# Performance work log

Hardware: AMD Instinct MI355X
Metric: run time of the kernel (lower is better)

Reference implementation:

```python
import jax, jax.numpy as jnp
import numpy as np

B, T, N, U = 64, 8, 1000, 64
IN_DIM = 1
F = IN_DIM + U          # per-node concat feature size = 65
K = 3                   # num_matrices = max_diffusion_step(2) * n_supports(1) + 1


def _scaled_laplacian(A):
    # calculate_scaled_laplacian from DCRNN preprocessing (filter_type='laplacian')
    A = np.maximum(A, A.T)
    d = A.sum(1)
    d_is = np.where(d > 0, d ** -0.5, 0.0)
    L = np.eye(N, dtype=np.float32) - (d_is[:, None] * A * d_is[None, :])
    lmax = float(np.linalg.eigvalsh(L).max())
    return ((2.0 / lmax) * L - np.eye(N, dtype=np.float32)).astype(np.float32)


def setup_inputs() -> dict:
    key = jax.random.key(0)
    ks = jax.random.split(key, 14)
    # sparse-ish random symmetric adjacency -> scaled Laplacian support
    mask = np.asarray(jax.random.uniform(ks[0], (N, N))) < 0.01
    A = (np.abs(np.asarray(jax.random.normal(ks[1], (N, N)))) * mask).astype(np.float32)
    support = jnp.asarray(_scaled_laplacian(A))

    s = 0.1
    inp = {
        'inputs': jax.random.normal(ks[2], (B, T, N), dtype=jnp.float32),
        'support': support,
        'enc_W_ru': jax.random.normal(ks[3], (F * K, 2 * U), dtype=jnp.float32) * s,
        'enc_b_ru': jnp.ones((2 * U,), jnp.float32),  # bias_start=1.0 in DCGRUCell
        'enc_W_c': jax.random.normal(ks[4], (F * K, U), dtype=jnp.float32) * s,
        'enc_b_c': jnp.zeros((U,), jnp.float32),
        'dec_W_ru': jax.random.normal(ks[5], (F * K, 2 * U), dtype=jnp.float32) * s,
        'dec_b_ru': jnp.ones((2 * U,), jnp.float32),
        'dec_W_c': jax.random.normal(ks[6], (F * K, U), dtype=jnp.float32) * s,
        'dec_b_c': jnp.zeros((U,), jnp.float32),
        'W_proj': jax.random.normal(ks[7], (U, 1), dtype=jnp.float32) * s,
        'b_proj': jnp.zeros((1,), jnp.float32),
    }
    return inp


def _gconv(S, x, h, W, b):
    # x: (B,N,in_dim), h: (B,N,U) -> diffusion conv with Chebyshev recurrence, K=3
    x0 = jnp.concatenate([x, h], axis=-1)                 # (B,N,F)
    x1 = jnp.einsum('mn,bnf->bmf', S, x0)
    x2 = 2.0 * jnp.einsum('mn,bnf->bmf', S, x1) - x0
    xs = jnp.stack([x0, x1, x2], axis=-1)                 # (B,N,F,K) -> matches torch f*K+k layout
    xs = xs.reshape(xs.shape[0], xs.shape[1], -1)         # (B,N,F*K)
    return jnp.einsum('bnf,fo->bno', xs, W) + b


def _dcgru_cell(S, x, h, W_ru, b_ru, W_c, b_c):
    ru = jax.nn.sigmoid(_gconv(S, x, h, W_ru, b_ru))      # (B,N,2U)
    r, u = jnp.split(ru, 2, axis=-1)
    c = jnp.tanh(_gconv(S, x, r * h, W_c, b_c))
    return u * h + (1.0 - u) * c


def reference(inputs, support, enc_W_ru, enc_b_ru, enc_W_c, enc_b_c,
              dec_W_ru, dec_b_ru, dec_W_c, dec_b_c, W_proj, b_proj):
    b, t, n = inputs.shape
    xseq = jnp.transpose(inputs, (1, 0, 2))[..., None]    # (T,B,N,1)
    h0 = jnp.zeros((b, n, U), inputs.dtype)

    def step(h, xt):
        h_new = _dcgru_cell(support, xt, h, enc_W_ru, enc_b_ru, enc_W_c, enc_b_c)
        return h_new, None

    h_enc, _ = jax.lax.scan(step, h0, xseq)
    # decoder: horizon=1, GO symbol = zeros
    go = jnp.zeros((b, n, 1), inputs.dtype)
    h_dec = _dcgru_cell(support, go, h_enc, dec_W_ru, dec_b_ru, dec_W_c, dec_b_c)
    out = (jnp.einsum('bnu,uo->bno', h_dec, W_proj) + b_proj)[..., 0]  # (B,N)
    return out
```

## Files before the change

### kernel.cpp

```cpp
#include <hip/hip_runtime.h>
#include <hip/hip_bf16.h>

namespace {
constexpr int B  = 64;
constexpr int T  = 8;
constexpr int N  = 1000;
constexpr int U  = 64;
constexpr int R  = B * N;
constexpr int RS = 256;
constexpr int CSR_CAP = 65536;
}

typedef short bf16x8 __attribute__((ext_vector_type(8)));
typedef float f32x4  __attribute__((ext_vector_type(4)));
typedef unsigned short u16;

__device__ __forceinline__ float bf2f(u16 x) {
  unsigned u = ((unsigned)x) << 16;
  float f; __builtin_memcpy(&f, &u, 4); return f;
}
__device__ __forceinline__ u16 f2bf(float f) {
  unsigned u; __builtin_memcpy(&u, &f, 4);
  u += 0x7FFFu + ((u >> 16) & 1u);
  return (u16)(u >> 16);
}


__global__ __launch_bounds__(256) void k_count(const float* __restrict__ S,
                                               int* __restrict__ rowptr) {
  int lane = threadIdx.x & 63;
  int m = blockIdx.x * 4 + (threadIdx.x >> 6);
  int c = 0;
  for (int n = lane; n < N; n += 64) c += (S[m * N + n] != 0.f) ? 1 : 0;
  for (int off = 32; off; off >>= 1) c += __shfl_down(c, off, 64);
  if (lane == 0) rowptr[m + 1] = c;
}

__global__ __launch_bounds__(1024) void k_scan(int* __restrict__ rowptr) {
  __shared__ int sm[1024];
  int t = threadIdx.x;
  sm[t] = (t < N) ? rowptr[t + 1] : 0;
  __syncthreads();
  for (int off = 1; off < 1024; off <<= 1) {
    int v = sm[t];
    int a = (t >= off) ? sm[t - off] : 0;
    __syncthreads();
    sm[t] = v + a;
    __syncthreads();
  }
  if (t < N) rowptr[t + 1] = sm[t];
  if (t == 0) rowptr[0] = 0;
}

__global__ __launch_bounds__(256) void k_fill(const float* __restrict__ S,
                                              const int* __restrict__ rowptr,
                                              int* __restrict__ cols,
                                              float* __restrict__ vals) {
  int lane = threadIdx.x & 63;
  int m = blockIdx.x * 4 + (threadIdx.x >> 6);
  int base = rowptr[m];
  for (int n0 = 0; n0 < N; n0 += 64) {
    int n = n0 + lane;
    float v = (n < N) ? S[m * N + n] : 0.f;
    bool nz = (v != 0.f);
    unsigned long long mask = __ballot(nz);
    int pos = base + (int)__popcll(mask & ((1ull << lane) - 1ull));
    if (nz && pos < CSR_CAP) { cols[pos] = n; vals[pos] = v; }
    base += (int)__popcll(mask);
  }
}


__global__ __launch_bounds__(256) void k_xt(const float* __restrict__ inp,
                                            float* __restrict__ xT) {
  __shared__ float tile[64][65];
  const int t  = blockIdx.y;
  const int n0 = blockIdx.x * 64;
  const int lx = threadIdx.x & 63;
  const int ly = threadIdx.x >> 6;
  for (int bb = ly; bb < 64; bb += 4) {
    int n = n0 + lx;
    tile[bb][lx] = (n < N) ? inp[(bb * T + t) * N + n] : 0.f;
  }
  __syncthreads();
  for (int nn = ly; nn < 64; nn += 4) {
    int n = n0 + nn;
    if (n < N) xT[((size_t)t * N + n) * 64 + lx] = tile[lx][nn];
  }
}


__global__ __launch_bounds__(64) void k_sspmv(const int* __restrict__ rowptr,
                                              const int* __restrict__ cols,
                                              const float* __restrict__ vals,
                                              const float* __restrict__ in,
                                              const float* __restrict__ sub,
                                              float* __restrict__ out, int cheb) {
  const int m = blockIdx.x, b = threadIdx.x;
  const size_t toff = (size_t)blockIdx.y * R;
  float acc = 0.f;
  for (int j = rowptr[m]; j < rowptr[m + 1]; ++j)
    acc = fmaf(vals[j], in[toff + cols[j] * 64 + b], acc);
  if (cheb) acc = 2.f * acc - sub[toff + m * 64 + b];
  out[toff + m * 64 + b] = acc;
}


__global__ __launch_bounds__(256) void k_wprep(
    const float* __restrict__ w0, const float* __restrict__ w1,
    const float* __restrict__ w2, const float* __restrict__ w3,
    u16* __restrict__ o0, u16* __restrict__ o1,
    u16* __restrict__ o2, u16* __restrict__ o3) {
  const float* W; u16* O; int ncol;
  switch (blockIdx.y) {
    case 0:  W = w0; O = o0; ncol = 128; break;
    case 1:  W = w1; O = o1; ncol = 64;  break;
    case 2:  W = w2; O = o2; ncol = 128; break;
    default: W = w3; O = o3; ncol = 64;  break;
  }
  int idx = blockIdx.x * 256 + threadIdx.x;
  if (idx >= ncol * RS) return;
  int o = idx / RS, kp = idx - o * RS;
  float v = 0.f;
  if (kp < 192)      v = W[(((kp & 63) + 1) * 3 + (kp >> 6)) * ncol + o];
  else if (kp < 195) v = W[(kp - 192) * ncol + o];
  O[idx] = f2bf(v);
}


__global__ __launch_bounds__(256) void k_zseg(u16* __restrict__ A) {
  int idx = blockIdx.x * 256 + threadIdx.x;
  int r = idx >> 3, q = idx & 7;
  bf16x8 z = {0, 0, 0, 0, 0, 0, 0, 0};
  *(bf16x8*)(A + (size_t)r * RS + q * 8) = z;
}


__global__ __launch_bounds__(256) void k_spv(
    const int* __restrict__ rowptr, const int* __restrict__ cols,
    const float* __restrict__ vals,
    const u16* __restrict__ in, const u16* __restrict__ sub,
    u16* __restrict__ out,
    const float* __restrict__ xs0, const float* __restrict__ xs1,
    const float* __restrict__ xs2,
    u16* __restrict__ scA, u16* __restrict__ scB, int xmode) {
  const int chunk = blockIdx.x;
  const int m = blockIdx.y * 4 + (threadIdx.x >> 6);
  const int l = threadIdx.x & 63;
  const int b = chunk * 8 + (l >> 3);
  const int cg = (l & 7) * 8;
  const int s = rowptr[m], e = rowptr[m + 1];

  float acc[8];
#pragma unroll
  for (int i = 0; i < 8; ++i) acc[i] = 0.f;

  int j = s;
  for (; j + 7 < e; j += 8) {
    float vv[8]; bf16x8 qq[8];
#pragma unroll
    for (int u8 = 0; u8 < 8; ++u8) {
      vv[u8] = vals[j + u8];
      qq[u8] = *(const bf16x8*)(in + ((size_t)cols[j + u8] * 64 + b) * RS + cg);
    }
#pragma unroll
    for (int i = 0; i < 8; ++i) {
      float a = acc[i];
#pragma unroll
      for (int u8 = 0; u8 < 8; ++u8) a = fmaf(vv[u8], bf2f((u16)qq[u8][i]), a);
      acc[i] = a;
    }
  }
  for (; j + 3 < e; j += 4) {
    const float v0 = vals[j],     v1 = vals[j + 1];
    const float v2 = vals[j + 2], v3 = vals[j + 3];
    bf16x8 q0 = *(const bf16x8*)(in + ((size_t)cols[j]     * 64 + b) * RS + cg);
    bf16x8 q1 = *(const bf16x8*)(in + ((size_t)cols[j + 1] * 64 + b) * RS + cg);
    bf16x8 q2 = *(const bf16x8*)(in + ((size_t)cols[j + 2] * 64 + b) * RS + cg);
    bf16x8 q3 = *(const bf16x8*)(in + ((size_t)cols[j + 3] * 64 + b) * RS + cg);
#pragma unroll
    for (int i = 0; i < 8; ++i)
      acc[i] = fmaf(v3, bf2f((u16)q3[i]),
               fmaf(v2, bf2f((u16)q2[i]),
               fmaf(v1, bf2f((u16)q1[i]),
               fmaf(v0, bf2f((u16)q0[i]), acc[i]))));
  }
  for (; j < e; ++j) {
    const float v = vals[j];
    bf16x8 q = *(const bf16x8*)(in + ((size_t)cols[j] * 64 + b) * RS + cg);
#pragma unroll
    for (int i = 0; i < 8; ++i) acc[i] = fmaf(v, bf2f((u16)q[i]), acc[i]);
  }

  const size_t ro = ((size_t)m * 64 + b) * RS + cg;
  if (sub) {
    bf16x8 sb = *(const bf16x8*)(sub + ro);
#pragma unroll
    for (int i = 0; i < 8; ++i) acc[i] = 2.f * acc[i] - bf2f((u16)sb[i]);
  }
  bf16x8 o;
#pragma unroll
  for (int i = 0; i < 8; ++i) o[i] = (short)f2bf(acc[i]);
  *(bf16x8*)(out + ro) = o;

  if (xmode && (l & 7) == 0) {
    const int r = m * 64 + b;
    u16 s0v = 0, s1v = 0, s2v = 0;
    if (xmode == 1) { s0v = f2bf(xs0[r]); s1v = f2bf(xs1[r]); s2v = f2bf(xs2[r]); }
    const size_t o2 = (size_t)r * RS + 192;
    scA[o2] = s0v; scA[o2 + 1] = s1v; scA[o2 + 2] = s2v;
    scB[o2] = s0v; scB[o2 + 1] = s1v; scB[o2 + 2] = s2v;
  }
}


template <int EPI>
__global__ __launch_bounds__(128) void k_mg2(
    const u16* __restrict__ A, const u16* __restrict__ Wt,
    const float* __restrict__ bias,
    u16* __restrict__ outA, u16* __restrict__ ubuf,
    float* __restrict__ hbuf) {
  __shared__ u16 Wl[64 * 128];
  const int chunk = blockIdx.x;
  const int ob = EPI ? 0 : blockIdx.z * 64;
  const int wv = threadIdx.x >> 6;
  const int n0 = EPI ? (blockIdx.y * 4 + wv * 2) : (blockIdx.y * 8 + wv * 4);
  const int l  = threadIdx.x & 63;
  const int lr = l & 15, lk = l >> 4;
  const int bphys = chunk * 8 + (lr & 7);
  const int tc = threadIdx.x & 15, tr0 = threadIdx.x >> 4;

  const size_t ra0 = ((size_t)(n0 + (lr >> 3)) * 64 + bphys) * RS + lk * 8;
  const size_t ra1 = ra0 + 2 * 64 * RS;

  f32x4 acc[2][4];
#pragma unroll
  for (int i = 0; i < 2; ++i)
#pragma unroll
    for (int j = 0; j < 4; ++j) acc[i][j] = (f32x4){0.f, 0.f, 0.f, 0.f};

  for (int r = tr0; r < 64; r += 8)
    *(bf16x8*)(Wl + r * 128 + ((tc ^ (r & 7)) * 8)) =
        *(const bf16x8*)(Wt + (size_t)(ob + r) * RS + tc * 8);
  __syncthreads();
#pragma unroll
  for (int ks = 0; ks < 4; ++ks) {
    bf16x8 a0 = *(const bf16x8*)(A + ra0 + ks * 32);
    bf16x8 a1;
    if (!EPI) a1 = *(const bf16x8*)(A + ra1 + ks * 32);
#pragma unroll
    for (int cb = 0; cb < 4; ++cb) {
      const int wrow = cb * 16 + lr;
      bf16x8 bb = *(const bf16x8*)(Wl + wrow * 128 +
                                   (((ks * 4 + lk) ^ (wrow & 7)) * 8));
      acc[0][cb] = __builtin_amdgcn_mfma_f32_16x16x32_bf16(a0, bb, acc[0][cb], 0, 0, 0);
      if (!EPI)
        acc[1][cb] = __builtin_amdgcn_mfma_f32_16x16x32_bf16(a1, bb, acc[1][cb], 0, 0, 0);
    }
  }
  __syncthreads();
  if (tc < 12)
    for (int r = tr0; r < 64; r += 8)
      *(bf16x8*)(Wl + r * 128 + ((tc ^ (r & 7)) * 8)) =
          *(const bf16x8*)(Wt + (size_t)(ob + r) * RS + 128 + tc * 8);
  __syncthreads();
#pragma unroll
  for (int ks = 4; ks < 7; ++ks) {
    bf16x8 a0 = *(const bf16x8*)(A + ra0 + ks * 32);
    bf16x8 a1;
    if (!EPI) a1 = *(const bf16x8*)(A + ra1 + ks * 32);
#pragma unroll
    for (int cb = 0; cb < 4; ++cb) {
      const int wrow = cb * 16 + lr;
      bf16x8 bb = *(const bf16x8*)(Wl + wrow * 128 +
                                   ((((ks - 4) * 4 + lk) ^ (wrow & 7)) * 8));
      acc[0][cb] = __builtin_amdgcn_mfma_f32_16x16x32_bf16(a0, bb, acc[0][cb], 0, 0, 0);
      if (!EPI)
        acc[1][cb] = __builtin_amdgcn_mfma_f32_16x16x32_bf16(a1, bb, acc[1][cb], 0, 0, 0);
    }
  }

#pragma unroll
  for (int mf = 0; mf < (EPI ? 1 : 2); ++mf)
#pragma unroll
    for (int cb = 0; cb < 4; ++cb) {
      const int col = ob + cb * 16 + lr;
      const float bs = bias[col];
#pragma unroll
      for (int j4 = 0; j4 < 4; ++j4) {
        const int trow = lk * 4 + j4;
        const int prow = (n0 + mf * 2 + (trow >> 3)) * 64 + chunk * 8 + (trow & 7);
        const float v = acc[mf][cb][j4] + bs;
        if (EPI == 0) {
          const float sig = 1.f / (1.f + expf(-v));
          if (col < 64)
            outA[(size_t)prow * RS + col] = f2bf(sig * hbuf[(size_t)prow * 64 + col]);
          else
            ubuf[(size_t)prow * 64 + (col - 64)] = f2bf(sig);
        } else {
          const float cc = tanhf(v);
          const size_t i64 = (size_t)prow * 64 + col;
          const float u = bf2f(ubuf[i64]);
          const float hn = u * hbuf[i64] + (1.f - u) * cc;
          hbuf[i64] = hn;
          outA[(size_t)prow * RS + col] = f2bf(hn);
        }
      }
    }
}


__global__ __launch_bounds__(256) void k_proj(const float* __restrict__ h,
                                              const float* __restrict__ Wp,
                                              const float* __restrict__ bp,
                                              float* __restrict__ out) {
  int lane = threadIdx.x & 63;
  int r = blockIdx.x * 4 + (threadIdx.x >> 6);
  float p = h[(size_t)r * 64 + lane] * Wp[lane];
  for (int off = 32; off; off >>= 1) p += __shfl_down(p, off, 64);
  if (lane == 0) {
    int n = r >> 6, b = r & 63;
    out[b * N + n] = p + bp[0];
  }
}


extern "C" void kernel_launch(void* const* d_in, const int* in_sizes, int n_in,
                              void* d_out, int out_size, void* d_ws, size_t ws_size,
                              hipStream_t stream) {
  const float* inp  = (const float*)d_in[0];
  const float* S    = (const float*)d_in[1];
  const float* eWru = (const float*)d_in[2];
  const float* ebru = (const float*)d_in[3];
  const float* eWc  = (const float*)d_in[4];
  const float* ebc  = (const float*)d_in[5];
  const float* dWru = (const float*)d_in[6];
  const float* dbru = (const float*)d_in[7];
  const float* dWc  = (const float*)d_in[8];
  const float* dbc  = (const float*)d_in[9];
  const float* Wp   = (const float*)d_in[10];
  const float* bp   = (const float*)d_in[11];
  float* out = (float*)d_out;

  char* p = (char*)d_ws;
  auto alloc = [&](size_t bytes) { void* q = p; p += (bytes + 255) & ~(size_t)255; return q; };
  u16*   A1    = (u16*)alloc((size_t)R * RS * 2);
  u16*   A2    = (u16*)alloc((size_t)R * RS * 2);
  float* hbuf  = (float*)alloc((size_t)R * 64 * 4);
  u16*   ubuf  = (u16*)alloc((size_t)R * 64 * 2);
  float* Xt    = (float*)alloc((size_t)T * R * 4);
  float* x1s   = (float*)alloc((size_t)T * R * 4);
  float* x2s   = (float*)alloc((size_t)T * R * 4);
  u16*   WtRUe = (u16*)alloc(128 * RS * 2);
  u16*   WtCe  = (u16*)alloc(64 * RS * 2);
  u16*   WtRUd = (u16*)alloc(128 * RS * 2);
  u16*   WtCd  = (u16*)alloc(64 * RS * 2);
  int*   rowptr = (int*)alloc(1024 * 4);
  int*   cols   = (int*)alloc(CSR_CAP * 4);
  float* vals   = (float*)alloc(CSR_CAP * 4);

  k_zseg<<<2000, 256, 0, stream>>>(A1);
  hipMemsetAsync(hbuf, 0, (size_t)R * 64 * 4, stream);

  k_count<<<250, 256, 0, stream>>>(S, rowptr);
  k_scan<<<1, 1024, 0, stream>>>(rowptr);
  k_fill<<<250, 256, 0, stream>>>(S, rowptr, cols, vals);
  k_xt<<<dim3(16, T), 256, 0, stream>>>(inp, Xt);
  k_sspmv<<<dim3(N, T), 64, 0, stream>>>(rowptr, cols, vals, Xt, nullptr, x1s, 0);
  k_sspmv<<<dim3(N, T), 64, 0, stream>>>(rowptr, cols, vals, x1s, Xt, x2s, 1);
  k_wprep<<<dim3(128, 4), 256, 0, stream>>>(eWru, eWc, dWru, dWc,
                                            WtRUe, WtCe, WtRUd, WtCd);

  dim3 gsp(8, 250);

  auto cell = [&](int t, const u16* Wru, const float* bru,
                  const u16* Wc, const float* bc) {
    const int xmode = (t >= 0) ? 1 : 2;
    const float* xs0 = (t >= 0) ? Xt  + (size_t)t * R : Xt;
    const float* xs1 = (t >= 0) ? x1s + (size_t)t * R : Xt;
    const float* xs2 = (t >= 0) ? x2s + (size_t)t * R : Xt;
    k_spv<<<gsp, 256, 0, stream>>>(rowptr, cols, vals, A1, nullptr, A1 + 64,
                                   xs0, xs1, xs2, A1, A2, xmode);
    k_spv<<<gsp, 256, 0, stream>>>(rowptr, cols, vals, A1 + 64, A1, A1 + 128,
                                   nullptr, nullptr, nullptr,
                                   nullptr, nullptr, 0);
    k_mg2<0><<<dim3(8, 125, 2), 128, 0, stream>>>(A1, Wru, bru, A2, ubuf, hbuf);
    k_spv<<<gsp, 256, 0, stream>>>(rowptr, cols, vals, A2, nullptr, A2 + 64,
                                   nullptr, nullptr, nullptr,
                                   nullptr, nullptr, 0);
    k_spv<<<gsp, 256, 0, stream>>>(rowptr, cols, vals, A2 + 64, A2, A2 + 128,
                                   nullptr, nullptr, nullptr,
                                   nullptr, nullptr, 0);
    k_mg2<1><<<dim3(8, 250), 128, 0, stream>>>(A2, Wc, bc, A1, ubuf, hbuf);
  };

  for (int t = 0; t < T; ++t) cell(t, WtRUe, ebru, WtCe, ebc);
  cell(-1, WtRUd, dbru, WtCd, dbc);

  k_proj<<<16000, 256, 0, stream>>>(hbuf, Wp, bp, out);
  (void)in_sizes; (void)n_in; (void)out_size; (void)ws_size;
}
```

Measured before the change: 960.4 us.

## Fuse second Chebyshev SpMV into the gate GEMM kernels via LDS staging

The second diffusion hop (2*S*x1 - x0) is now computed inside the GEMM kernel and written to shared memory, where it feeds the MFMA K-slices directly. This removes a separate SpMV launch per gconv and the global write and read of the x2 segment. Weights are now read straight from global or cache instead of being staged in LDS, and the RU GEMM covers all 128 outputs in one block rather than splitting across blockIdx.z. The cost is that the SpMV gather now runs inside the GEMM block and may lower occupancy or overlap.

```diff
diff --git a/kernel.cpp b/kernel.cpp
--- a/kernel.cpp
+++ b/kernel.cpp
@@ -138,9 +138,7 @@
 
 __global__ __launch_bounds__(256) void k_spv(
     const int* __restrict__ rowptr, const int* __restrict__ cols,
-    const float* __restrict__ vals,
-    const u16* __restrict__ in, const u16* __restrict__ sub,
-    u16* __restrict__ out,
+    const float* __restrict__ vals, u16* __restrict__ A,
     const float* __restrict__ xs0, const float* __restrict__ xs1,
     const float* __restrict__ xs2,
     u16* __restrict__ scA, u16* __restrict__ scB, int xmode) {
@@ -155,6 +153,7 @@
 #pragma unroll
   for (int i = 0; i < 8; ++i) acc[i] = 0.f;
 
+  const u16* in = A;
   int j = s;
   for (; j + 7 < e; j += 8) {
     float vv[8]; bf16x8 qq[8];
@@ -192,16 +191,11 @@
     for (int i = 0; i < 8; ++i) acc[i] = fmaf(v, bf2f((u16)q[i]), acc[i]);
   }
 
-  const size_t ro = ((size_t)m * 64 + b) * RS + cg;
-  if (sub) {
-    bf16x8 sb = *(const bf16x8*)(sub + ro);
-#pragma unroll
-    for (int i = 0; i < 8; ++i) acc[i] = 2.f * acc[i] - bf2f((u16)sb[i]);
-  }
+  const size_t ro = ((size_t)m * 64 + b) * RS + 64 + cg;
   bf16x8 o;
 #pragma unroll
   for (int i = 0; i < 8; ++i) o[i] = (short)f2bf(acc[i]);
-  *(bf16x8*)(out + ro) = o;
+  *(bf16x8*)(A + ro) = o;
 
   if (xmode && (l & 7) == 0) {
     const int r = m * 64 + b;
@@ -215,98 +209,141 @@
 
 
 template <int EPI>
-__global__ __launch_bounds__(128) void k_mg2(
+__global__ __launch_bounds__(256) void k_mgf(
+    const int* __restrict__ rowptr, const int* __restrict__ cols,
+    const float* __restrict__ vals,
     const u16* __restrict__ A, const u16* __restrict__ Wt,
     const float* __restrict__ bias,
     u16* __restrict__ outA, u16* __restrict__ ubuf,
     float* __restrict__ hbuf) {
-  __shared__ u16 Wl[64 * 128];
+  constexpr int NF = EPI ? 4 : 8;
+  __shared__ u16 X2[64 * 64];
   const int chunk = blockIdx.x;
-  const int ob = EPI ? 0 : blockIdx.z * 64;
-  const int wv = threadIdx.x >> 6;
-  const int n0 = EPI ? (blockIdx.y * 4 + wv * 2) : (blockIdx.y * 8 + wv * 4);
-  const int l  = threadIdx.x & 63;
-  const int lr = l & 15, lk = l >> 4;
-  const int bphys = chunk * 8 + (lr & 7);
-  const int tc = threadIdx.x & 15, tr0 = threadIdx.x >> 4;
-
-  const size_t ra0 = ((size_t)(n0 + (lr >> 3)) * 64 + bphys) * RS + lk * 8;
-  const size_t ra1 = ra0 + 2 * 64 * RS;
-
-  f32x4 acc[2][4];
-#pragma unroll
-  for (int i = 0; i < 2; ++i)
-#pragma unroll
-    for (int j = 0; j < 4; ++j) acc[i][j] = (f32x4){0.f, 0.f, 0.f, 0.f};
-
-  for (int r = tr0; r < 64; r += 8)
-    *(bf16x8*)(Wl + r * 128 + ((tc ^ (r & 7)) * 8)) =
-        *(const bf16x8*)(Wt + (size_t)(ob + r) * RS + tc * 8);
-  __syncthreads();
-#pragma unroll
-  for (int ks = 0; ks < 4; ++ks) {
-    bf16x8 a0 = *(const bf16x8*)(A + ra0 + ks * 32);
-    bf16x8 a1;
-    if (!EPI) a1 = *(const bf16x8*)(A + ra1 + ks * 32);
-#pragma unroll
-    for (int cb = 0; cb < 4; ++cb) {
-      const int wrow = cb * 16 + lr;
-      bf16x8 bb = *(const bf16x8*)(Wl + wrow * 128 +
-                                   (((ks * 4 + lk) ^ (wrow & 7)) * 8));
-      acc[0][cb] = __builtin_amdgcn_mfma_f32_16x16x32_bf16(a0, bb, acc[0][cb], 0, 0, 0);
-      if (!EPI)
-        acc[1][cb] = __builtin_amdgcn_mfma_f32_16x16x32_bf16(a1, bb, acc[1][cb], 0, 0, 0);
-    }
-  }
-  __syncthreads();
-  if (tc < 12)
-    for (int r = tr0; r < 64; r += 8)
-      *(bf16x8*)(Wl + r * 128 + ((tc ^ (r & 7)) * 8)) =
-          *(const bf16x8*)(Wt + (size_t)(ob + r) * RS + 128 + tc * 8);
-  __syncthreads();
-#pragma unroll
-  for (int ks = 4; ks < 7; ++ks) {
-    bf16x8 a0 = *(const bf16x8*)(A + ra0 + ks * 32);
-    bf16x8 a1;
-    if (!EPI) a1 = *(const bf16x8*)(A + ra1 + ks * 32);
-#pragma unroll
-    for (int cb = 0; cb < 4; ++cb) {
-      const int wrow = cb * 16 + lr;
-      bf16x8 bb = *(const bf16x8*)(Wl + wrow * 128 +
-                                   ((((ks - 4) * 4 + lk) ^ (wrow & 7)) * 8));
-      acc[0][cb] = __builtin_amdgcn_mfma_f32_16x16x32_bf16(a0, bb, acc[0][cb], 0, 0, 0);
-      if (!EPI)
-        acc[1][cb] = __builtin_amdgcn_mfma_f32_16x16x32_bf16(a1, bb, acc[1][cb], 0, 0, 0);
-    }
-  }
-
-#pragma unroll
-  for (int mf = 0; mf < (EPI ? 1 : 2); ++mf)
-#pragma unroll
-    for (int cb = 0; cb < 4; ++cb) {
-      const int col = ob + cb * 16 + lr;
-      const float bs = bias[col];
-#pragma unroll
-      for (int j4 = 0; j4 < 4; ++j4) {
-        const int trow = lk * 4 + j4;
-        const int prow = (n0 + mf * 2 + (trow >> 3)) * 64 + chunk * 8 + (trow & 7);
-        const float v = acc[mf][cb][j4] + bs;
-        if (EPI == 0) {
-          const float sig = 1.f / (1.f + expf(-v));
-          if (col < 64)
-            outA[(size_t)prow * RS + col] = f2bf(sig * hbuf[(size_t)prow * 64 + col]);
-          else
-            ubuf[(size_t)prow * 64 + (col - 64)] = f2bf(sig);
-        } else {
-          const float cc = tanhf(v);
-          const size_t i64 = (size_t)prow * 64 + col;
-          const float u = bf2f(ubuf[i64]);
-          const float hn = u * hbuf[i64] + (1.f - u) * cc;
-          hbuf[i64] = hn;
-          outA[(size_t)prow * RS + col] = f2bf(hn);
+  const int w = threadIdx.x >> 6;
+  const int l = threadIdx.x & 63;
+  const int n0b = blockIdx.y * 8;
+
+  {
+    const int bl = l >> 3, cg8 = l & 7;
+    const int bphys = chunk * 8 + bl;
+    const u16* in = A + 64;
+    const int cg = cg8 * 8;
+#pragma unroll
+    for (int nl2 = 0; nl2 < 2; ++nl2) {
+      const int n = n0b + w * 2 + nl2;
+      const int s = rowptr[n], e = rowptr[n + 1];
+      float acc[8];
+#pragma unroll
+      for (int i = 0; i < 8; ++i) acc[i] = 0.f;
+      int j = s;
+      for (; j + 7 < e; j += 8) {
+        float vv[8]; bf16x8 qq[8];
+#pragma unroll
+        for (int u8 = 0; u8 < 8; ++u8) {
+          vv[u8] = vals[j + u8];
+          qq[u8] = *(const bf16x8*)(in + ((size_t)cols[j + u8] * 64 + bphys) * RS + cg);
+        }
+#pragma unroll
+        for (int i = 0; i < 8; ++i) {
+          float a = acc[i];
+#pragma unroll
+          for (int u8 = 0; u8 < 8; ++u8) a = fmaf(vv[u8], bf2f((u16)qq[u8][i]), a);
+          acc[i] = a;
         }
       }
-    }
+      for (; j + 3 < e; j += 4) {
+        const float v0 = vals[j],     v1 = vals[j + 1];
+        const float v2 = vals[j + 2], v3 = vals[j + 3];
+        bf16x8 q0 = *(const bf16x8*)(in + ((size_t)cols[j]     * 64 + bphys) * RS + cg);
+        bf16x8 q1 = *(const bf16x8*)(in + ((size_t)cols[j + 1] * 64 + bphys) * RS + cg);
+        bf16x8 q2 = *(const bf16x8*)(in + ((size_t)cols[j + 2] * 64 + bphys) * RS + cg);
+        bf16x8 q3 = *(const bf16x8*)(in + ((size_t)cols[j + 3] * 64 + bphys) * RS + cg);
+#pragma unroll
+        for (int i = 0; i < 8; ++i)
+          acc[i] = fmaf(v3, bf2f((u16)q3[i]),
+                   fmaf(v2, bf2f((u16)q2[i]),
+                   fmaf(v1, bf2f((u16)q1[i]),
+                   fmaf(v0, bf2f((u16)q0[i]), acc[i]))));
+      }
+      for (; j < e; ++j) {
+        const float v = vals[j];
+        bf16x8 q = *(const bf16x8*)(in + ((size_t)cols[j] * 64 + bphys) * RS + cg);
+#pragma unroll
+        for (int i = 0; i < 8; ++i) acc[i] = fmaf(v, bf2f((u16)q[i]), acc[i]);
+      }
+      bf16x8 x0 = *(const bf16x8*)(A + ((size_t)n * 64 + bphys) * RS + cg);
+      bf16x8 o;
+#pragma unroll
+      for (int i = 0; i < 8; ++i) o[i] = (short)f2bf(2.f * acc[i] - bf2f((u16)x0[i]));
+      const int rloc = (w * 2 + nl2) * 8 + bl;
+      *(bf16x8*)(X2 + rloc * 64 + ((cg8 ^ bl) * 8)) = o;
+    }
+  }
+  __syncthreads();
+
+  const int lr = l & 15, lk = l >> 4;
+  const size_t ra = ((size_t)(n0b + w * 2 + (lr >> 3)) * 64 +
+                     chunk * 8 + (lr & 7)) * RS + lk * 8;
+  const u16* pw = Wt + (size_t)lr * RS + lk * 8;
+
+  f32x4 acc[NF];
+#pragma unroll
+  for (int cb = 0; cb < NF; ++cb) acc[cb] = (f32x4){0.f, 0.f, 0.f, 0.f};
+
+#pragma unroll
+  for (int ks = 0; ks < 4; ++ks) {
+    bf16x8 a = *(const bf16x8*)(A + ra + ks * 32);
+#pragma unroll
+    for (int cb = 0; cb < NF; ++cb) {
+      bf16x8 bb = *(const bf16x8*)(pw + (size_t)cb * (16 * RS) + ks * 32);
+      acc[cb] = __builtin_amdgcn_mfma_f32_16x16x32_bf16(a, bb, acc[cb], 0, 0, 0);
+    }
+  }
+  const int rloc = w * 16 + lr;
+#pragma unroll
+  for (int k2 = 0; k2 < 2; ++k2) {
+    bf16x8 a = *(const bf16x8*)(X2 + rloc * 64 + (((k2 * 4 + lk) ^ (lr & 7)) * 8));
+    const int ks = 4 + k2;
+#pragma unroll
+    for (int cb = 0; cb < NF; ++cb) {
+      bf16x8 bb = *(const bf16x8*)(pw + (size_t)cb * (16 * RS) + ks * 32);
+      acc[cb] = __builtin_amdgcn_mfma_f32_16x16x32_bf16(a, bb, acc[cb], 0, 0, 0);
+    }
+  }
+  {
+    bf16x8 a = *(const bf16x8*)(A + ra + 6 * 32);
+#pragma unroll
+    for (int cb = 0; cb < NF; ++cb) {
+      bf16x8 bb = *(const bf16x8*)(pw + (size_t)cb * (16 * RS) + 6 * 32);
+      acc[cb] = __builtin_amdgcn_mfma_f32_16x16x32_bf16(a, bb, acc[cb], 0, 0, 0);
+    }
+  }
+
+#pragma unroll
+  for (int cb = 0; cb < NF; ++cb) {
+    const int col = cb * 16 + lr;
+    const float bs = bias[col];
+#pragma unroll
+    for (int j4 = 0; j4 < 4; ++j4) {
+      const int trow = lk * 4 + j4;
+      const int prow = (n0b + w * 2 + (trow >> 3)) * 64 + chunk * 8 + (trow & 7);
+      const float v = acc[cb][j4] + bs;
+      if (EPI == 0) {
+        const float sig = 1.f / (1.f + expf(-v));
+        if (col < 64)
+          outA[(size_t)prow * RS + col] = f2bf(sig * hbuf[(size_t)prow * 64 + col]);
+        else
+          ubuf[(size_t)prow * 64 + (col - 64)] = f2bf(sig);
+      } else {
+        const float cc = tanhf(v);
+        const size_t i64 = (size_t)prow * 64 + col;
+        const float u = bf2f(ubuf[i64]);
+        const float hn = u * hbuf[i64] + (1.f - u) * cc;
+        hbuf[i64] = hn;
+        outA[(size_t)prow * RS + col] = f2bf(hn);
+      }
+    }
+  }
 }
 
 
@@ -372,6 +409,7 @@
                                             WtRUe, WtCe, WtRUd, WtCd);
 
   dim3 gsp(8, 250);
+  dim3 gsm(8, 125);
 
   auto cell = [&](int t, const u16* Wru, const float* bru,
                   const u16* Wc, const float* bc) {
@@ -379,19 +417,15 @@
     const float* xs0 = (t >= 0) ? Xt  + (size_t)t * R : Xt;
     const float* xs1 = (t >= 0) ? x1s + (size_t)t * R : Xt;
     const float* xs2 = (t >= 0) ? x2s + (size_t)t * R : Xt;
-    k_spv<<<gsp, 256, 0, stream>>>(rowptr, cols, vals, A1, nullptr, A1 + 64,
+    k_spv<<<gsp, 256, 0, stream>>>(rowptr, cols, vals, A1,
                                    xs0, xs1, xs2, A1, A2, xmode);
-    k_spv<<<gsp, 256, 0, stream>>>(rowptr, cols, vals, A1 + 64, A1, A1 + 128,
+    k_mgf<0><<<gsm, 256, 0, stream>>>(rowptr, cols, vals, A1, Wru, bru,
+                                      A2, ubuf, hbuf);
+    k_spv<<<gsp, 256, 0, stream>>>(rowptr, cols, vals, A2,
                                    nullptr, nullptr, nullptr,
                                    nullptr, nullptr, 0);
-    k_mg2<0><<<dim3(8, 125, 2), 128, 0, stream>>>(A1, Wru, bru, A2, ubuf, hbuf);
-    k_spv<<<gsp, 256, 0, stream>>>(rowptr, cols, vals, A2, nullptr, A2 + 64,
-                                   nullptr, nullptr, nullptr,
-                                   nullptr, nullptr, 0);
-    k_spv<<<gsp, 256, 0, stream>>>(rowptr, cols, vals, A2 + 64, A2, A2 + 128,
-                                   nullptr, nullptr, nullptr,
-                                   nullptr, nullptr, 0);
-    k_mg2<1><<<dim3(8, 250), 128, 0, stream>>>(A2, Wc, bc, A1, ubuf, hbuf);
+    k_mgf<1><<<gsm, 256, 0, stream>>>(rowptr, cols, vals, A2, Wc, bc,
+                                      A1, ubuf, hbuf);
   };
 
   for (int t = 0; t < T; ++t) cell(t, WtRUe, ebru, WtCe, ebc);
```

New measurement: 1.108 ms. 1.15x slower.
